# Performance work log

Measured on AMD Instinct MI355X. Metric: run time of the kernel, lower is better.

Reference implementation:

```python
import jax, jax.numpy as jnp
import numpy as np

DIM = 64
NUM_EXPERTS = 4
TOP_K = 2


def _dwconv3x3(x, w, b):
    # x: [B, C, H, W], w: [C, 1, 3, 3] depthwise (groups=C), b: [C]
    y = jax.lax.conv_general_dilated(
        x, w, window_strides=(1, 1), padding='SAME',
        feature_group_count=x.shape[1],
        dimension_numbers=('NCHW', 'OIHW', 'NCHW'))
    return y + b[None, :, None, None]


def setup_inputs() -> dict:
    key = jax.random.key(0)
    ks = jax.random.split(key, 12)
    B, H, W = 8, 128, 128
    s = 0.02
    return {
        'x': jax.random.normal(ks[0], (B, 2 * DIM, H, W), jnp.float32),
        'pre_w': jax.random.normal(ks[1], (DIM, 2 * DIM), jnp.float32) * s,
        'pre_b': jax.random.normal(ks[2], (DIM,), jnp.float32) * s,
        'gate_w0': jax.random.normal(ks[3], (NUM_EXPERTS, DIM), jnp.float32) * s,
        'gate_b0': jax.random.normal(ks[4], (NUM_EXPERTS,), jnp.float32) * s,
        'gate_w1': jax.random.normal(ks[5], (NUM_EXPERTS, DIM), jnp.float32) * s,
        'gate_b1': jax.random.normal(ks[6], (NUM_EXPERTS,), jnp.float32) * s,
        'exp_w1': jax.random.normal(ks[7], (NUM_EXPERTS, DIM, 1, 3, 3), jnp.float32) * s,
        'exp_b1': jax.random.normal(ks[8], (NUM_EXPERTS, DIM), jnp.float32) * s,
        'exp_w2': jax.random.normal(ks[9], (NUM_EXPERTS, DIM, 1, 3, 3), jnp.float32) * s,
        'exp_b2': jax.random.normal(ks[10], (NUM_EXPERTS, DIM), jnp.float32) * s,
    }


def reference(x, pre_w, pre_b, gate_w0, gate_b0, gate_w1, gate_b1,
              exp_w1, exp_b1, exp_w2, exp_b2):
    # pre_fuse: 1x1 conv [2*dim -> dim]
    x = jnp.einsum('bchw,oc->bohw', x, pre_w) + pre_b[None, :, None, None]

    # --- GateNetwork ---
    pooled = jnp.max(x, axis=(2, 3)) + jnp.mean(x, axis=(2, 3))  # [B, dim]
    logits = jax.nn.leaky_relu(pooled @ gate_w1.T + gate_b1, 0.2)  # [B, E]
    noise = jax.nn.softplus(pooled @ gate_w0.T + gate_b0)          # [B, E]
    n_mean = jnp.mean(noise, axis=1, keepdims=True)
    n_std = jnp.std(noise, axis=1, keepdims=True, ddof=1)          # unbiased like torch.std
    scores = logits + (noise - n_mean) / n_std
    _, topk_idx = jax.lax.top_k(scores, TOP_K)                     # [B, k]
    B = logits.shape[0]
    mask = jnp.zeros_like(logits).at[jnp.arange(B)[:, None], topk_idx].set(1.0)
    masked = jnp.where(mask > 0, logits, -jnp.inf)
    cof = jax.nn.softmax(masked, axis=1)                           # [B, E]

    # --- experts: dwconv3x3 -> GELU -> dwconv3x3, combined by gating coeffs ---
    def expert_fn(w1, b1, w2, b2):
        h = _dwconv3x3(x, w1, b1)
        h = jax.nn.gelu(h, approximate=False)
        return _dwconv3x3(h, w2, b2)

    outs = jax.vmap(expert_fn)(exp_w1, exp_b1, exp_w2, exp_b2)     # [E, B, dim, H, W]
    out = jnp.einsum('ebchw,be->bchw', outs, cof)
    return out
```

## Files before the change

kernel.cpp:

```cpp
#include <hip/hip_runtime.h>
#include <hip/hip_bf16.h>
#include <math.h>

#define HW 16384
#define IMG 128
#define C_IN 128
#define C_OUT 64
#define NB 8
#define NE 4

typedef __attribute__((ext_vector_type(8))) short bf16x8;
typedef __attribute__((ext_vector_type(4))) float f32x4;

static __device__ __forceinline__ float bf2f_u(unsigned hbits) {
  union { unsigned u; float f; } v; v.u = hbits << 16;
  return v.f;
}
static __device__ __forceinline__ float bf2f_hi(unsigned w) {
  union { unsigned u; float f; } v; v.u = w & 0xFFFF0000u;
  return v.f;
}
static __device__ __forceinline__ unsigned cvtpk(float a, float b) {
  __hip_bfloat162 p = __float22bfloat162_rn(make_float2(a, b));
  union { __hip_bfloat162 h; unsigned u; } v; v.h = p;
  return v.u;
}
static __device__ __forceinline__ void pk2(float a, float b,
                                           unsigned& hi, unsigned& lo) {
  hi = cvtpk(a, b);
  float ra = a - bf2f_u(hi & 0xFFFFu);
  float rb = b - bf2f_u(hi >> 16);
  lo = cvtpk(ra, rb);
}

union FragU { unsigned u[4]; uint4 q; bf16x8 v; };

#define ASYNC_LOAD16(gsrc, ldst)                                              \
  __builtin_amdgcn_global_load_lds(                                           \
      (const __attribute__((address_space(1))) void*)(gsrc),                  \
      (__attribute__((address_space(3))) void*)(ldst), 16, 0, 0)

__global__ __launch_bounds__(64, 4) void prefuse_mfma(
    const float* __restrict__ x, const float* __restrict__ pre_w,
    const float* __restrict__ pre_b, unsigned short* __restrict__ x1,
    float* __restrict__ pmax, float* __restrict__ psum) {
  __shared__ float xls[3][1056];
  __shared__ unsigned short tbuf[16][72];
  int lane = threadIdx.x;
  int rowb = lane & 15;
  int kg = lane >> 4;
  int blk = blockIdx.x;
  int b = blk >> 9;
  int strip = blk & 511;
  int px0 = strip << 5;

  const float* xbase = x + (size_t)b * C_IN * HW + px0;

#define STAGE(ks, bf)                                                         \
  {                                                                           \
    _Pragma("unroll")                                                         \
    for (int r = 0; r < 4; ++r) {                                             \
      int ch = (ks) * 32 + r * 8 + (lane >> 3);                               \
      ASYNC_LOAD16(xbase + (size_t)ch * HW + (lane & 7) * 4,                  \
                   &xls[bf][r * 264]);                                        \
    }                                                                         \
  }

  STAGE(0, 0)
  STAGE(1, 1)

  f32x4 acc[2][4];
#pragma unroll
  for (int ot = 0; ot < 4; ++ot) {
    float t = pre_b[ot * 16 + rowb];
#pragma unroll
    for (int pt = 0; pt < 2; ++pt) acc[pt][ot] = (f32x4){t, t, t, t};
  }

#pragma unroll
  for (int k = 0; k < 4; ++k) {
    FragU wh[4], wl[4];
#pragma unroll
    for (int ot = 0; ot < 4; ++ot) {
      const float* wp = pre_w + (ot * 16 + rowb) * C_IN + k * 32 + kg * 8;
      float4 a = *(const float4*)wp;
      float4 cq = *(const float4*)(wp + 4);
      pk2(a.x, a.y, wh[ot].u[0], wl[ot].u[0]);
      pk2(a.z, a.w, wh[ot].u[1], wl[ot].u[1]);
      pk2(cq.x, cq.y, wh[ot].u[2], wl[ot].u[2]);
      pk2(cq.z, cq.w, wh[ot].u[3], wl[ot].u[3]);
    }
    if (k < 2) {
      STAGE(k + 2, (k + 2) % 3)
      asm volatile("s_waitcnt vmcnt(8)" ::: "memory");
    } else if (k == 2) {
      asm volatile("s_waitcnt vmcnt(8)" ::: "memory");
    } else {
      asm volatile("s_waitcnt vmcnt(0)" ::: "memory");
    }
    const float* xb = xls[k % 3];
#pragma unroll
    for (int pt = 0; pt < 2; ++pt) {
      float xv[8];
#pragma unroll
      for (int j = 0; j < 8; ++j)
        xv[j] = xb[kg * 264 + j * 32 + pt * 16 + rowb];
      FragU h, l;
      pk2(xv[0], xv[1], h.u[0], l.u[0]);
      pk2(xv[2], xv[3], h.u[1], l.u[1]);
      pk2(xv[4], xv[5], h.u[2], l.u[2]);
      pk2(xv[6], xv[7], h.u[3], l.u[3]);
#pragma unroll
      for (int ot = 0; ot < 4; ++ot) {
        acc[pt][ot] = __builtin_amdgcn_mfma_f32_16x16x32_bf16(h.v, wh[ot].v, acc[pt][ot], 0, 0, 0);
        acc[pt][ot] = __builtin_amdgcn_mfma_f32_16x16x32_bf16(l.v, wh[ot].v, acc[pt][ot], 0, 0, 0);
        acc[pt][ot] = __builtin_amdgcn_mfma_f32_16x16x32_bf16(h.v, wl[ot].v, acc[pt][ot], 0, 0, 0);
      }
    }
  }
#undef STAGE

#pragma unroll
  for (int ot = 0; ot < 4; ++ot) {
    float m = -INFINITY, s = 0.f;
#pragma unroll
    for (int pt = 0; pt < 2; ++pt)
#pragma unroll
      for (int r = 0; r < 4; ++r) {
        float v = acc[pt][ot][r];
        m = fmaxf(m, v); s += v;
      }
    m = fmaxf(m, __shfl_xor(m, 16)); s += __shfl_xor(s, 16);
    m = fmaxf(m, __shfl_xor(m, 32)); s += __shfl_xor(s, 32);
    if (lane < 16) {
      int idx = strip * 512 + b * 64 + ot * 16 + lane;
      pmax[idx] = m; psum[idx] = s;
    }
#pragma unroll
    for (int pt = 0; pt < 2; ++pt) {
      uint2 p;
      p.x = cvtpk(acc[pt][ot][0], acc[pt][ot][1]);
      p.y = cvtpk(acc[pt][ot][2], acc[pt][ot][3]);
      *(uint2*)&tbuf[rowb][pt * 16 + kg * 4] = p;
    }
    __syncthreads();
    uint4 val = *(const uint4*)&tbuf[lane >> 2][(lane & 3) * 8];
    unsigned short* op = x1 + ((size_t)b * C_OUT + ot * 16 + (lane >> 2)) * HW
                            + px0 + (lane & 3) * 8;
    *(uint4*)op = val;
    __syncthreads();
  }
}

__global__ __launch_bounds__(1024) void pool_gate_kernel(
    const float* __restrict__ pmax, const float* __restrict__ psum,
    const float* __restrict__ gw0, const float* __restrict__ gb0,
    const float* __restrict__ gw1, const float* __restrict__ gb1,
    float* __restrict__ cof) {
  __shared__ float rm[16][64], rs[16][64], pooled[64];
  int b = blockIdx.x;
  int t = threadIdx.x;
  int o = t & 63, g = t >> 6;
  float m = -INFINITY, s = 0.f;
#pragma unroll
  for (int i = 0; i < 32; ++i) {
    int idx = (g * 32 + i) * 512 + b * 64 + o;
    m = fmaxf(m, pmax[idx]);
    s += psum[idx];
  }
  rm[g][o] = m; rs[g][o] = s;
  __syncthreads();
  if (t < 64) {
    float mm = rm[0][t], ss = rs[0][t];
#pragma unroll
    for (int g2 = 1; g2 < 16; ++g2) {
      mm = fmaxf(mm, rm[g2][t]);
      ss += rs[g2][t];
    }
    pooled[t] = mm + ss * (1.0f / HW);

    int lane = t;
    float pv = pooled[lane];
    float acc[8];
#pragma unroll
    for (int e = 0; e < NE; ++e) {
      acc[e]     = pv * gw0[e * C_OUT + lane];
      acc[4 + e] = pv * gw1[e * C_OUT + lane];
    }
#pragma unroll
    for (int d = 32; d >= 1; d >>= 1)
#pragma unroll
      for (int q = 0; q < 8; ++q) acc[q] += __shfl_xor(acc[q], d);

    if (lane == 0) {
      float logits[NE], noise[NE];
#pragma unroll
      for (int e = 0; e < NE; ++e) {
        float d0 = acc[e] + gb0[e];
        float d1 = acc[4 + e] + gb1[e];
        logits[e] = d1 > 0.f ? d1 : 0.2f * d1;
        noise[e] = log1pf(expf(d0));
      }
      float mn = 0.25f * (noise[0] + noise[1] + noise[2] + noise[3]);
      float var = 0.f;
#pragma unroll
      for (int e = 0; e < NE; ++e) { float d = noise[e] - mn; var += d * d; }
      float sd = sqrtf(var * (1.0f / 3.0f));
      float scores[NE];
#pragma unroll
      for (int e = 0; e < NE; ++e) scores[e] = logits[e] + (noise[e] - mn) / sd;
      int i0 = 0;
#pragma unroll
      for (int e = 1; e < NE; ++e) if (scores[e] > scores[i0]) i0 = e;
      int i1 = -1;
#pragma unroll
      for (int e = 0; e < NE; ++e)
        if (e != i0 && (i1 < 0 || scores[e] > scores[i1])) i1 = e;
      float mm2 = fmaxf(logits[i0], logits[i1]);
      float e0 = expf(logits[i0] - mm2), e1 = expf(logits[i1] - mm2);
      float inv = 1.0f / (e0 + e1);
#pragma unroll
      for (int e = 0; e < NE; ++e) cof[b * NE + e] = 0.f;
      cof[b * NE + i0] = e0 * inv;
      cof[b * NE + i1] = e1 * inv;
    }
  }
}

__global__ __launch_bounds__(256) void expert_kernel(
    const unsigned short* __restrict__ x1, const float* __restrict__ ew1,
    const float* __restrict__ eb1, const float* __restrict__ ew2,
    const float* __restrict__ eb2, const float* __restrict__ cof,
    float* __restrict__ out) {
  __shared__ float xs[36][132];
  int tid = threadIdx.x, blk = blockIdx.x;
  int rt = blk & 3;
  int c = (blk >> 2) & 63;
  int b = blk >> 8;
  int ty0 = rt * 32;
  const unsigned short* xp = x1 + ((size_t)b * C_OUT + c) * HW;

  int eA = -1, eB = -1; float cfA = 0.f, cfB = 0.f;
#pragma unroll
  for (int e = 0; e < NE; ++e) {
    float cv = cof[b * NE + e];
    if (cv != 0.f) { if (eA < 0) { eA = e; cfA = cv; } else { eB = e; cfB = cv; } }
  }
  if (eA < 0) { eA = 0; cfA = 0.f; }
  if (eB < 0) { eB = eA; cfB = 0.f; }

  float w1A[9], w1B[9], w2A[9], w2B[9];
#pragma unroll
  for (int t = 0; t < 9; ++t) {
    w1A[t] = ew1[((size_t)eA * C_OUT + c) * 9 + t];
    w1B[t] = ew1[((size_t)eB * C_OUT + c) * 9 + t];
    w2A[t] = cfA * ew2[((size_t)eA * C_OUT + c) * 9 + t];
    w2B[t] = cfB * ew2[((size_t)eB * C_OUT + c) * 9 + t];
  }
  float b1A = eb1[eA * C_OUT + c], b1B = eb1[eB * C_OUT + c];
  float bias2 = cfA * eb2[eA * C_OUT + c] + cfB * eb2[eB * C_OUT + c];

  for (int i = tid; i < 36 * 16; i += 256) {
    int r = i >> 4, seg = i & 15;
    int gy = ty0 - 2 + r;
    float4 f0 = make_float4(0.f, 0.f, 0.f, 0.f), f1 = f0;
    if ((unsigned)gy < 128u) {
      uint4 u = *(const uint4*)(xp + gy * IMG + seg * 8);
      f0.x = bf2f_u(u.x); f0.y = bf2f_hi(u.x);
      f0.z = bf2f_u(u.y); f0.w = bf2f_hi(u.y);
      f1.x = bf2f_u(u.z); f1.y = bf2f_hi(u.z);
      f1.z = bf2f_u(u.w); f1.w = bf2f_hi(u.w);
    }
    float* row = &xs[r][8 * seg];
    *(float2*)(row + 2) = make_float2(f0.x, f0.y);
    *(float4*)(row + 4) = make_float4(f0.z, f0.w, f1.x, f1.y);
    *(float2*)(row + 8) = make_float2(f1.z, f1.w);
  }
  if (tid < 36) {
    xs[tid][0] = 0.f; xs[tid][1] = 0.f; xs[tid][130] = 0.f; xs[tid][131] = 0.f;
  }
  __syncthreads();

  int pr = tid >> 5, pc = tid & 31;
  int px0 = pc * 4;
  int xrb = pr * 4;

  float acc[4][4];
#pragma unroll
  for (int r = 0; r < 4; ++r)
#pragma unroll
    for (int cc = 0; cc < 4; ++cc) acc[r][cc] = bias2;

  float X[3][8];
#define LOADROW(slot, rr)                                                     \
  {                                                                           \
    const float* xr = &xs[rr][px0];                                           \
    float4 a = *(const float4*)xr;                                            \
    float4 bb = *(const float4*)(xr + 4);                                     \
    X[slot][0] = a.x;  X[slot][1] = a.y;  X[slot][2] = a.z;  X[slot][3] = a.w;\
    X[slot][4] = bb.x; X[slot][5] = bb.y; X[slot][6] = bb.z; X[slot][7] = bb.w;\
  }
  LOADROW(0, xrb)
  LOADROW(1, xrb + 1)

#pragma unroll
  for (int k = 0; k < 6; ++k) {
    LOADROW((k + 2) % 3, xrb + k + 2)
    bool rowok = (unsigned)(ty0 + pr * 4 - 1 + k) < 128u;
    float hA[6], hB[6];
#pragma unroll
    for (int j = 0; j < 6; ++j) {
      float sA = b1A, sB = b1B;
#pragma unroll
      for (int dy = 0; dy < 3; ++dy) {
        const float* xw = X[(k + dy) % 3];
#pragma unroll
        for (int dx = 0; dx < 3; ++dx) {
          float xv = xw[j + dx];
          sA = fmaf(xv, w1A[dy * 3 + dx], sA);
          sB = fmaf(xv, w1B[dy * 3 + dx], sB);
        }
      }
      float uA = sA * sA, uB = sB * sB;
      float tA = fmaf(uA, fmaf(uA, 0.025f, -0.16666667f), 1.0f);
      float tB = fmaf(uB, fmaf(uB, 0.025f, -0.16666667f), 1.0f);
      float gA = sA * fmaf(0.3989422804f * sA, tA, 0.5f);
      float gB = sB * fmaf(0.3989422804f * sB, tB, 0.5f);
      bool ok = rowok && ((unsigned)(px0 - 1 + j) < 128u);
      hA[j] = ok ? gA : 0.f;
      hB[j] = ok ? gB : 0.f;
    }
#pragma unroll
    for (int dy = 0; dy < 3; ++dy) {
      int r = k - dy;
      if (r >= 0 && r < 4) {
#pragma unroll
        for (int cc = 0; cc < 4; ++cc) {
          float a = acc[r][cc];
          a = fmaf(hA[cc],     w2A[dy * 3 + 0], a);
          a = fmaf(hA[cc + 1], w2A[dy * 3 + 1], a);
          a = fmaf(hA[cc + 2], w2A[dy * 3 + 2], a);
          a = fmaf(hB[cc],     w2B[dy * 3 + 0], a);
          a = fmaf(hB[cc + 1], w2B[dy * 3 + 1], a);
          a = fmaf(hB[cc + 2], w2B[dy * 3 + 2], a);
          acc[r][cc] = a;
        }
      }
    }
  }
#undef LOADROW

  float* op = out + ((size_t)b * C_OUT + c) * HW + (ty0 + pr * 4) * IMG + px0;
#pragma unroll
  for (int r = 0; r < 4; ++r)
    *(float4*)(op + r * IMG) = make_float4(acc[r][0], acc[r][1], acc[r][2], acc[r][3]);
}

extern "C" void kernel_launch(void* const* d_in, const int* in_sizes, int n_in,
                              void* d_out, int out_size, void* d_ws, size_t ws_size,
                              hipStream_t stream) {
  const float* x     = (const float*)d_in[0];
  const float* pre_w = (const float*)d_in[1];
  const float* pre_b = (const float*)d_in[2];
  const float* gw0   = (const float*)d_in[3];
  const float* gb0   = (const float*)d_in[4];
  const float* gw1   = (const float*)d_in[5];
  const float* gb1   = (const float*)d_in[6];
  const float* ew1   = (const float*)d_in[7];
  const float* eb1   = (const float*)d_in[8];
  const float* ew2   = (const float*)d_in[9];
  const float* eb2   = (const float*)d_in[10];
  float* out = (float*)d_out;

  char* ws = (char*)d_ws;
  unsigned short* x1 = (unsigned short*)ws;
  float* pmax = (float*)(ws + 16777216);
  float* psum = (float*)(ws + 17825792);
  float* cof  = (float*)(ws + 18874368);

  prefuse_mfma<<<4096, 64, 0, stream>>>(x, pre_w, pre_b, x1, pmax, psum);
  pool_gate_kernel<<<8, 1024, 0, stream>>>(pmax, psum, gw0, gb0, gw1, gb1, cof);
  expert_kernel<<<2048, 256, 0, stream>>>(x1, ew1, eb1, ew2, eb2, cof, out);
}
```

Before: 70.25 us.

## Stage whole bf16 plane per expert block and deepen prefuse prefetch to four stages

The expert kernel now loads one full 128x128 bf16 channel plane into shared memory, keeping it as bf16 with a 2-pixel shift and zero halo rows. Each block then loops over the four row tiles, so the halo rows between tiles are no longer reloaded and the grid drops from 2048 to 512 blocks. Separately, the prefuse kernel issues all four K-stage async loads up front into four LDS buffers and relaxes its waitcnts. The trade-offs are fewer blocks for latency hiding (512 blocks of 256 threads), about 36KB of LDS per expert block, and bf16-to-fp32 unpacking in the inner loop.

```diff
diff --git a/kernel.cpp b/kernel.cpp
--- a/kernel.cpp
+++ b/kernel.cpp
@@ -44,7 +44,7 @@
     const float* __restrict__ x, const float* __restrict__ pre_w,
     const float* __restrict__ pre_b, unsigned short* __restrict__ x1,
     float* __restrict__ pmax, float* __restrict__ psum) {
-  __shared__ float xls[3][1056];
+  __shared__ float xls[4][1056];
   __shared__ unsigned short tbuf[16][72];
   int lane = threadIdx.x;
   int rowb = lane & 15;
@@ -68,6 +68,7 @@
 
   STAGE(0, 0)
   STAGE(1, 1)
+  STAGE(2, 2)
 
   f32x4 acc[2][4];
 #pragma unroll
@@ -90,15 +91,17 @@
       pk2(cq.x, cq.y, wh[ot].u[2], wl[ot].u[2]);
       pk2(cq.z, cq.w, wh[ot].u[3], wl[ot].u[3]);
     }
-    if (k < 2) {
-      STAGE(k + 2, (k + 2) % 3)
+    if (k == 0) {
+      STAGE(3, 3)
+      asm volatile("s_waitcnt vmcnt(12)" ::: "memory");
+    } else if (k == 1) {
       asm volatile("s_waitcnt vmcnt(8)" ::: "memory");
     } else if (k == 2) {
-      asm volatile("s_waitcnt vmcnt(8)" ::: "memory");
+      asm volatile("s_waitcnt vmcnt(4)" ::: "memory");
     } else {
       asm volatile("s_waitcnt vmcnt(0)" ::: "memory");
     }
-    const float* xb = xls[k % 3];
+    const float* xb = xls[k];
 #pragma unroll
     for (int pt = 0; pt < 2; ++pt) {
       float xv[8];
@@ -232,12 +235,9 @@
     const float* __restrict__ eb1, const float* __restrict__ ew2,
     const float* __restrict__ eb2, const float* __restrict__ cof,
     float* __restrict__ out) {
-  __shared__ float xs[36][132];
+  __shared__ unsigned short xs[132][136];
   int tid = threadIdx.x, blk = blockIdx.x;
-  int rt = blk & 3;
-  int c = (blk >> 2) & 63;
-  int b = blk >> 8;
-  int ty0 = rt * 32;
+  int c = blk & 63, b = blk >> 6;
   const unsigned short* xp = x1 + ((size_t)b * C_OUT + c) * HW;
 
   int eA = -1, eB = -1; float cfA = 0.f, cfB = 0.f;
@@ -260,100 +260,102 @@
   float b1A = eb1[eA * C_OUT + c], b1B = eb1[eB * C_OUT + c];
   float bias2 = cfA * eb2[eA * C_OUT + c] + cfB * eb2[eB * C_OUT + c];
 
-  for (int i = tid; i < 36 * 16; i += 256) {
-    int r = i >> 4, seg = i & 15;
-    int gy = ty0 - 2 + r;
-    float4 f0 = make_float4(0.f, 0.f, 0.f, 0.f), f1 = f0;
-    if ((unsigned)gy < 128u) {
-      uint4 u = *(const uint4*)(xp + gy * IMG + seg * 8);
-      f0.x = bf2f_u(u.x); f0.y = bf2f_hi(u.x);
-      f0.z = bf2f_u(u.y); f0.w = bf2f_hi(u.y);
-      f1.x = bf2f_u(u.z); f1.y = bf2f_hi(u.z);
-      f1.z = bf2f_u(u.w); f1.w = bf2f_hi(u.w);
-    }
-    float* row = &xs[r][8 * seg];
-    *(float2*)(row + 2) = make_float2(f0.x, f0.y);
-    *(float4*)(row + 4) = make_float4(f0.z, f0.w, f1.x, f1.y);
-    *(float2*)(row + 8) = make_float2(f1.z, f1.w);
-  }
-  if (tid < 36) {
-    xs[tid][0] = 0.f; xs[tid][1] = 0.f; xs[tid][130] = 0.f; xs[tid][131] = 0.f;
+  for (int i = tid; i < 128 * 17; i += 256) {
+    int r = i / 17, j = i - r * 17;
+    uint4 cur = make_uint4(0u, 0u, 0u, 0u);
+    if (j < 16) cur = *(const uint4*)(xp + r * IMG + j * 8);
+    unsigned prevw = (j > 0) ? ((const uint4*)(xp + r * IMG + (j - 1) * 8))->w : 0u;
+    uint4 o; o.x = prevw; o.y = cur.x; o.z = cur.y; o.w = cur.z;
+    *(uint4*)&xs[r + 2][j * 8] = o;
+  }
+  for (int i = tid; i < 4 * 17; i += 256) {
+    int rr = i / 17, j = i - rr * 17;
+    int r = (rr < 2) ? rr : 128 + rr;
+    *(uint4*)&xs[r][j * 8] = make_uint4(0u, 0u, 0u, 0u);
   }
   __syncthreads();
 
   int pr = tid >> 5, pc = tid & 31;
   int px0 = pc * 4;
-  int xrb = pr * 4;
-
-  float acc[4][4];
-#pragma unroll
-  for (int r = 0; r < 4; ++r)
-#pragma unroll
-    for (int cc = 0; cc < 4; ++cc) acc[r][cc] = bias2;
 
   float X[3][8];
-#define LOADROW(slot, rr)                                                     \
+#define LOADROW(slot, rowidx)                                                 \
   {                                                                           \
-    const float* xr = &xs[rr][px0];                                           \
-    float4 a = *(const float4*)xr;                                            \
-    float4 bb = *(const float4*)(xr + 4);                                     \
-    X[slot][0] = a.x;  X[slot][1] = a.y;  X[slot][2] = a.z;  X[slot][3] = a.w;\
-    X[slot][4] = bb.x; X[slot][5] = bb.y; X[slot][6] = bb.z; X[slot][7] = bb.w;\
-  }
-  LOADROW(0, xrb)
-  LOADROW(1, xrb + 1)
-
-#pragma unroll
-  for (int k = 0; k < 6; ++k) {
-    LOADROW((k + 2) % 3, xrb + k + 2)
-    bool rowok = (unsigned)(ty0 + pr * 4 - 1 + k) < 128u;
-    float hA[6], hB[6];
-#pragma unroll
-    for (int j = 0; j < 6; ++j) {
-      float sA = b1A, sB = b1B;
+    const unsigned short* xr = &xs[rowidx][px0];                              \
+    uint2 a = *(const uint2*)xr;                                              \
+    uint2 bq = *(const uint2*)(xr + 4);                                       \
+    X[slot][0] = bf2f_u(a.x & 0xFFFFu);  X[slot][1] = bf2f_hi(a.x);           \
+    X[slot][2] = bf2f_u(a.y & 0xFFFFu);  X[slot][3] = bf2f_hi(a.y);           \
+    X[slot][4] = bf2f_u(bq.x & 0xFFFFu); X[slot][5] = bf2f_hi(bq.x);          \
+    X[slot][6] = bf2f_u(bq.y & 0xFFFFu); X[slot][7] = bf2f_hi(bq.y);          \
+  }
+
+#pragma unroll 1
+  for (int rt = 0; rt < 4; ++rt) {
+    int ty0 = rt * 32;
+    int xrb = ty0 + pr * 4;
+
+    float acc[4][4];
+#pragma unroll
+    for (int r = 0; r < 4; ++r)
+#pragma unroll
+      for (int cc = 0; cc < 4; ++cc) acc[r][cc] = bias2;
+
+    LOADROW(0, xrb)
+    LOADROW(1, xrb + 1)
+
+#pragma unroll
+    for (int k = 0; k < 6; ++k) {
+      LOADROW((k + 2) % 3, xrb + k + 2)
+      bool rowok = (unsigned)(ty0 + pr * 4 - 1 + k) < 128u;
+      float hA[6], hB[6];
+#pragma unroll
+      for (int j = 0; j < 6; ++j) {
+        float sA = b1A, sB = b1B;
+#pragma unroll
+        for (int dy = 0; dy < 3; ++dy) {
+          const float* xw = X[(k + dy) % 3];
+#pragma unroll
+          for (int dx = 0; dx < 3; ++dx) {
+            float xv = xw[j + dx];
+            sA = fmaf(xv, w1A[dy * 3 + dx], sA);
+            sB = fmaf(xv, w1B[dy * 3 + dx], sB);
+          }
+        }
+        float uA = sA * sA, uB = sB * sB;
+        float tA = fmaf(uA, fmaf(uA, 0.025f, -0.16666667f), 1.0f);
+        float tB = fmaf(uB, fmaf(uB, 0.025f, -0.16666667f), 1.0f);
+        float gA = sA * fmaf(0.3989422804f * sA, tA, 0.5f);
+        float gB = sB * fmaf(0.3989422804f * sB, tB, 0.5f);
+        bool ok = rowok && ((unsigned)(px0 - 1 + j) < 128u);
+        hA[j] = ok ? gA : 0.f;
+        hB[j] = ok ? gB : 0.f;
+      }
 #pragma unroll
       for (int dy = 0; dy < 3; ++dy) {
-        const float* xw = X[(k + dy) % 3];
-#pragma unroll
-        for (int dx = 0; dx < 3; ++dx) {
-          float xv = xw[j + dx];
-          sA = fmaf(xv, w1A[dy * 3 + dx], sA);
-          sB = fmaf(xv, w1B[dy * 3 + dx], sB);
+        int r = k - dy;
+        if (r >= 0 && r < 4) {
+#pragma unroll
+          for (int cc = 0; cc < 4; ++cc) {
+            float a = acc[r][cc];
+            a = fmaf(hA[cc],     w2A[dy * 3 + 0], a);
+            a = fmaf(hA[cc + 1], w2A[dy * 3 + 1], a);
+            a = fmaf(hA[cc + 2], w2A[dy * 3 + 2], a);
+            a = fmaf(hB[cc],     w2B[dy * 3 + 0], a);
+            a = fmaf(hB[cc + 1], w2B[dy * 3 + 1], a);
+            a = fmaf(hB[cc + 2], w2B[dy * 3 + 2], a);
+            acc[r][cc] = a;
+          }
         }
       }
-      float uA = sA * sA, uB = sB * sB;
-      float tA = fmaf(uA, fmaf(uA, 0.025f, -0.16666667f), 1.0f);
-      float tB = fmaf(uB, fmaf(uB, 0.025f, -0.16666667f), 1.0f);
-      float gA = sA * fmaf(0.3989422804f * sA, tA, 0.5f);
-      float gB = sB * fmaf(0.3989422804f * sB, tB, 0.5f);
-      bool ok = rowok && ((unsigned)(px0 - 1 + j) < 128u);
-      hA[j] = ok ? gA : 0.f;
-      hB[j] = ok ? gB : 0.f;
-    }
-#pragma unroll
-    for (int dy = 0; dy < 3; ++dy) {
-      int r = k - dy;
-      if (r >= 0 && r < 4) {
-#pragma unroll
-        for (int cc = 0; cc < 4; ++cc) {
-          float a = acc[r][cc];
-          a = fmaf(hA[cc],     w2A[dy * 3 + 0], a);
-          a = fmaf(hA[cc + 1], w2A[dy * 3 + 1], a);
-          a = fmaf(hA[cc + 2], w2A[dy * 3 + 2], a);
-          a = fmaf(hB[cc],     w2B[dy * 3 + 0], a);
-          a = fmaf(hB[cc + 1], w2B[dy * 3 + 1], a);
-          a = fmaf(hB[cc + 2], w2B[dy * 3 + 2], a);
-          acc[r][cc] = a;
-        }
-      }
-    }
+    }
+
+    float* op = out + ((size_t)b * C_OUT + c) * HW + (ty0 + pr * 4) * IMG + px0;
+#pragma unroll
+    for (int r = 0; r < 4; ++r)
+      *(float4*)(op + r * IMG) = make_float4(acc[r][0], acc[r][1], acc[r][2], acc[r][3]);
   }
 #undef LOADROW
-
-  float* op = out + ((size_t)b * C_OUT + c) * HW + (ty0 + pr * 4) * IMG + px0;
-#pragma unroll
-  for (int r = 0; r < 4; ++r)
-    *(float4*)(op + r * IMG) = make_float4(acc[r][0], acc[r][1], acc[r][2], acc[r][3]);
 }
 
 extern "C" void kernel_launch(void* const* d_in, const int* in_sizes, int n_in,
@@ -380,5 +382,5 @@
 
   prefuse_mfma<<<4096, 64, 0, stream>>>(x, pre_w, pre_b, x1, pmax, psum);
   pool_gate_kernel<<<8, 1024, 0, stream>>>(pmax, psum, gw0, gb0, gw1, gb1, cof);
-  expert_kernel<<<2048, 256, 0, stream>>>(x1, ew1, eb1, ew2, eb2, cof, out);
-}
+  expert_kernel<<<512, 256, 0, stream>>>(x1, ew1, eb1, ew2, eb2, cof, out);
+}
```

New measurement: 71.47 us. Within noise of the previous version (+1.7%).
